# Optimization experiments

Hardware: AMD Instinct MI355X
Metric: run time of the kernel (lower is better)

Reference implementation:

```python
import jax, jax.numpy as jnp
import numpy as np

B = 131072
D = 64          # d_model
T = 4           # num_tiles
TEMP = 0.5


def setup_inputs() -> dict:
    key = jax.random.key(0)
    ks = jax.random.split(key, 16)
    s = 0.02
    return {
        "a_vec": jax.random.normal(ks[0], (B, D), dtype=jnp.float32),
        "b_vec": jax.random.normal(ks[1], (B, D), dtype=jnp.float32),
        "pos_encoding": jax.random.normal(ks[2], (B, 8), dtype=jnp.float32),
        # router: Linear(2D+8 -> D), GELU, Linear(D -> T)
        "Wr1": jax.random.normal(ks[3], (2 * D + 8, D), dtype=jnp.float32) * s,
        "br1": jnp.zeros((D,), dtype=jnp.float32),
        "Wr2": jax.random.normal(ks[4], (D, T), dtype=jnp.float32) * s,
        "br2": jnp.zeros((T,), dtype=jnp.float32),
        # tile nets: per-tile Linear(2D -> 2D), GELU, Linear(2D -> D)
        "W1": jax.random.normal(ks[5], (T, 2 * D, 2 * D), dtype=jnp.float32) * s,
        "b1": jnp.zeros((T, 2 * D), dtype=jnp.float32),
        "W2": jax.random.normal(ks[6], (T, 2 * D, D), dtype=jnp.float32) * s,
        "b2": jnp.zeros((T, D), dtype=jnp.float32),
    }


def _router(x, Wr1, br1, Wr2, br2):
    h = jax.nn.gelu(x @ Wr1 + br1, approximate=False)  # torch nn.GELU is exact
    return (h @ Wr2 + br2) / TEMP


def reference(a_vec, b_vec, pos_encoding, Wr1, br1, Wr2, br2, W1, b1, W2, b2):
    pair = jnp.concatenate([a_vec, b_vec], axis=-1)            # (B, 2D)

    # Routing 1 uses pair; routing 2 uses flipped pair. Both expert passes
    # consume `pair` (faithful to the original code, which feeds pair both times).
    idx1 = jnp.argmax(_router(jnp.concatenate([pair, pos_encoding], -1),
                              Wr1, br1, Wr2, br2), axis=-1)    # (B,)
    pair_flip = jnp.concatenate([b_vec, a_vec], axis=-1)
    idx2 = jnp.argmax(_router(jnp.concatenate([pair_flip, pos_encoding], -1),
                              Wr1, br1, Wr2, br2), axis=-1)    # (B,)

    # Run all tiles on every sample (small T), then gather the routed output.
    h = jax.nn.gelu(jnp.einsum('bi,tij->btj', pair, W1) + b1, approximate=False)  # (B,T,2D)
    out_all = jnp.einsum('bth,thd->btd', h, W2) + b2                              # (B,T,D)

    out1 = jnp.take_along_axis(out_all, idx1[:, None, None], axis=1)[:, 0]
    out2 = jnp.take_along_axis(out_all, idx2[:, None, None], axis=1)[:, 0]
    return out1, out2
```

## Files before the change

kernel.cpp:

```cpp
#include <hip/hip_runtime.h>

#define B_N 131072

using bfrag_t = __attribute__((ext_vector_type(8))) short;
using acc_t   = __attribute__((ext_vector_type(4))) float;
using v4f     = __attribute__((ext_vector_type(4))) float;
using i32x4_t = __attribute__((ext_vector_type(4))) int;

__device__ __forceinline__ unsigned short f2bf(float f) {
  unsigned int u = __float_as_uint(f);
  u += 0x7FFFu + ((u >> 16) & 1u);
  return (unsigned short)(u >> 16);
}

__device__ __forceinline__ unsigned int pk2bf(float x, float y) {
  return (unsigned int)f2bf(x) | ((unsigned int)f2bf(y) << 16);
}

__device__ __forceinline__ void gload_lds16(const void* g, void* l) {
  __builtin_amdgcn_global_load_lds((const __attribute__((address_space(1))) void*)g,
                                   (__attribute__((address_space(3))) void*)l, 16, 0, 0);
}

__device__ __forceinline__ float gelu_f(float x) {
  float ax = fabsf(x) * 0.70710678118654752f;
  float t  = __builtin_amdgcn_rcpf(fmaf(0.3275911f, ax, 1.0f));
  float p  = fmaf(1.061405429f, t, -1.453152027f);
  p = fmaf(p, t, 1.421413741f);
  p = fmaf(p, t, -0.284496736f);
  p = fmaf(p, t, 0.254829592f);
  p = p * t;
  float e  = __expf(-ax * ax);
  float er = fmaf(-p, e, 1.0f);
  er = (x < 0.0f) ? -er : er;
  return 0.5f * x * (1.0f + er);
}

__global__ __launch_bounds__(256) void prepack2_k(
    const float* __restrict__ Wr1, const float* __restrict__ br1,
    const float* __restrict__ Wr2, const float* __restrict__ br2,
    const float* __restrict__ W1, const float* __restrict__ W2,
    float* __restrict__ RW, short* __restrict__ W1s, short* __restrict__ W2s,
    unsigned int* __restrict__ counts) {
  int gt = blockIdx.x * 256 + threadIdx.x;
  if (gt < 4) counts[gt] = 0u;
  for (int idx = gt; idx < 142 * 64; idx += 16384) {
    int row = idx >> 6, j = idx & 63; float val;
    if (row < 136)      val = Wr1[row * 64 + j];
    else if (row == 136) val = br1[j];
    else if (row < 141) val = Wr2[(row - 137) * 64 + j];
    else                val = (j < 4) ? br2[j] : 0.0f;
    RW[idx] = val;
  }
  for (int ch = gt; ch < 8192; ch += 16384) {
    int t = ch >> 11, r = (ch >> 4) & 127, c = ch & 15;
    const float* src = W1 + t * 16384 + r;
    short* dst = W1s + (t * 128 + r) * 128 + ((c ^ (r & 15)) * 8);
    #pragma unroll
    for (int m = 0; m < 8; m++) dst[m] = (short)f2bf(src[(c * 8 + m) * 128]);
  }
  for (int ch = gt; ch < 4096; ch += 16384) {
    int t = ch >> 10, d = (ch >> 4) & 63, c = ch & 15;
    const float* src = W2 + t * 8192 + d;
    short* dst = W2s + (t * 64 + d) * 128 + ((c ^ (d & 15)) * 8);
    #pragma unroll
    for (int m = 0; m < 8; m++) dst[m] = (short)f2bf(src[(c * 8 + m) * 64]);
  }
}

__global__ __launch_bounds__(256) void router7_k(
    const float* __restrict__ a, const float* __restrict__ b,
    const float* __restrict__ pos, const float* __restrict__ RW,
    unsigned char* __restrict__ r1, unsigned char* __restrict__ r2,
    unsigned int* __restrict__ gcounts) {
  __shared__ float SB[17928];
  __shared__ unsigned int hcnt[4];
  const int XA = 9088, XB = 13248, PP = 17408;
  int tid = threadIdx.x, wave = tid >> 6, lane = tid & 63;
  int s0 = blockIdx.x * 64;
  if (tid < 4) hcnt[tid] = 0u;

  for (int it = 0; it < 9; it++) {
    int cb = it * 256 + wave * 64;
    if (cb < 2272) {
      int chunk = cb + lane;
      if (chunk < 2272) gload_lds16(RW + chunk * 4, (char*)SB + cb * 16);
    }
  }
  #pragma unroll
  for (int it = 0; it < 4; it++) {
    int idx = it * 256 + tid;
    int s = idx >> 4, c = idx & 15;
    v4f va = *(const v4f*)(a + (size_t)(s0 + s) * 64 + c * 4);
    v4f vb = *(const v4f*)(b + (size_t)(s0 + s) * 64 + c * 4);
    #pragma unroll
    for (int k = 0; k < 4; k++) {
      SB[XA + (c * 4 + k) * 65 + s] = va[k];
      SB[XB + (c * 4 + k) * 65 + s] = vb[k];
    }
  }
  #pragma unroll
  for (int r = 0; r < 2; r++) {
    int idx = r * 256 + tid;
    int s = idx >> 3, c = idx & 7;
    SB[PP + c * 65 + s] = pos[(size_t)(s0 + s) * 8 + c];
  }
  __syncthreads();

  int sq = tid >> 2, jq = tid & 3;
  v4f acc1[4], acc2[4];
  #pragma unroll
  for (int e = 0; e < 4; e++) {
    v4f bi = *(const v4f*)(SB + 136 * 64 + jq * 16 + e * 4);
    acc1[e] = bi; acc2[e] = bi;
  }
  #pragma unroll 4
  for (int i = 0; i < 64; ++i) {
    float xa = SB[XA + i * 65 + sq];
    float xb = SB[XB + i * 65 + sq];
    const v4f* w = (const v4f*)(SB + i * 64 + jq * 16);
    v4f xav = {xa, xa, xa, xa}, xbv = {xb, xb, xb, xb};
    #pragma unroll
    for (int e = 0; e < 4; e++) {
      v4f wv = w[e];
      acc1[e] = __builtin_elementwise_fma(xav, wv, acc1[e]);
      acc2[e] = __builtin_elementwise_fma(xbv, wv, acc2[e]);
    }
  }
  #pragma unroll 4
  for (int i = 0; i < 64; ++i) {
    float xa = SB[XA + i * 65 + sq];
    float xb = SB[XB + i * 65 + sq];
    const v4f* w = (const v4f*)(SB + (64 + i) * 64 + jq * 16);
    v4f xav = {xa, xa, xa, xa}, xbv = {xb, xb, xb, xb};
    #pragma unroll
    for (int e = 0; e < 4; e++) {
      v4f wv = w[e];
      acc1[e] = __builtin_elementwise_fma(xbv, wv, acc1[e]);
      acc2[e] = __builtin_elementwise_fma(xav, wv, acc2[e]);
    }
  }
  #pragma unroll 2
  for (int i = 0; i < 8; ++i) {
    float p = SB[PP + i * 65 + sq];
    const v4f* w = (const v4f*)(SB + (128 + i) * 64 + jq * 16);
    v4f pv = {p, p, p, p};
    #pragma unroll
    for (int e = 0; e < 4; e++) {
      v4f wv = w[e];
      acc1[e] = __builtin_elementwise_fma(pv, wv, acc1[e]);
      acc2[e] = __builtin_elementwise_fma(pv, wv, acc2[e]);
    }
  }
  #pragma unroll
  for (int e = 0; e < 4; e++) {
    #pragma unroll
    for (int c = 0; c < 4; c++) {
      acc1[e][c] = gelu_f(acc1[e][c]);
      acc2[e][c] = gelu_f(acc2[e][c]);
    }
  }
  __syncthreads();
  #pragma unroll
  for (int e = 0; e < 4; e++) {
    #pragma unroll
    for (int c = 0; c < 4; c++) {
      int j = jq * 16 + e * 4 + c;
      SB[XA + j * 65 + sq] = acc1[e][c];
      SB[XB + j * 65 + sq] = acc2[e][c];
    }
  }
  __syncthreads();
  v4f l1 = *(const v4f*)(SB + 141 * 64);
  v4f l2 = l1;
  #pragma unroll 4
  for (int j = 0; j < 64; ++j) {
    float h1 = SB[XA + j * 65 + sq];
    float h2 = SB[XB + j * 65 + sq];
    v4f w2 = *(const v4f*)(SB + 137 * 64 + j * 4);
    v4f h1v = {h1, h1, h1, h1}, h2v = {h2, h2, h2, h2};
    l1 = __builtin_elementwise_fma(h1v, w2, l1);
    l2 = __builtin_elementwise_fma(h2v, w2, l2);
  }
  int idx1 = 0; float b1v = l1[0];
  if (l1[1] > b1v) { b1v = l1[1]; idx1 = 1; }
  if (l1[2] > b1v) { b1v = l1[2]; idx1 = 2; }
  if (l1[3] > b1v) { b1v = l1[3]; idx1 = 3; }
  int idx2 = 0; float b2v = l2[0];
  if (l2[1] > b2v) { b2v = l2[1]; idx2 = 1; }
  if (l2[2] > b2v) { b2v = l2[2]; idx2 = 2; }
  if (l2[3] > b2v) { b2v = l2[3]; idx2 = 3; }
  if (jq == 0) {
    r1[s0 + sq] = (unsigned char)idx1;
    r2[s0 + sq] = (unsigned char)idx2;
    atomicAdd(&hcnt[idx1], 1u);
    atomicAdd(&hcnt[idx2], 1u);
  }
  __syncthreads();
  if (tid < 4) atomicAdd(&gcounts[tid], hcnt[tid]);
}

__global__ __launch_bounds__(256) void offsets_k(
    const unsigned int* __restrict__ counts, unsigned int* __restrict__ table,
    unsigned int* __restrict__ cursors, unsigned int* __restrict__ list) {
  __shared__ unsigned int ps[5], cnt[4];
  int tid = threadIdx.x;
  if (tid == 0) {
    unsigned int acc = 0;
    for (int t = 0; t < 4; t++) {
      ps[t] = acc;
      unsigned int c = counts[t];
      cnt[t] = c;
      acc += ((c + 127u) >> 7) << 7;
    }
    ps[4] = acc;
    #pragma unroll
    for (int t = 0; t < 5; t++) table[t] = ps[t];
    #pragma unroll
    for (int t = 0; t < 4; t++) cursors[t] = ps[t];
  }
  __syncthreads();
  #pragma unroll
  for (int r = 0; r < 2; r++) {
    int idx = r * 256 + tid;
    int t = idx >> 7, i = idx & 127;
    unsigned int pos = ps[t] + cnt[t] + (unsigned int)i;
    if (pos < ps[t + 1]) list[pos] = 0xFFFFFFFFu;
  }
}

__global__ __launch_bounds__(256) void place_k(
    const unsigned char* __restrict__ r1, const unsigned char* __restrict__ r2,
    unsigned int* __restrict__ cursors, unsigned int* __restrict__ list) {
  __shared__ unsigned int lc[4], lb[4];
  int tid = threadIdx.x;
  if (tid < 4) lc[tid] = 0u;
  __syncthreads();
  int s = blockIdx.x * 256 + tid;
  int e1 = (int)r1[s], e2 = (int)r2[s];
  unsigned int k1 = atomicAdd(&lc[e1], 1u);
  unsigned int k2 = atomicAdd(&lc[e2], 1u);
  __syncthreads();
  if (tid < 4) lb[tid] = atomicAdd(&cursors[tid], lc[tid]);
  __syncthreads();
  list[lb[e1] + k1] = ((unsigned int)s << 1);
  list[lb[e2] + k2] = ((unsigned int)s << 1) | 1u;
}

__global__ __launch_bounds__(256) void expert3_k(
    const float* __restrict__ a, const float* __restrict__ b,
    const short* __restrict__ W1s, const short* __restrict__ W2s,
    const float* __restrict__ b1, const float* __restrict__ b2,
    const unsigned int* __restrict__ table, const unsigned int* __restrict__ list,
    float* __restrict__ out) {
  __shared__ short LB[24576];
  __shared__ unsigned int eLS[128];
  int tid = threadIdx.x;
  int wave = tid >> 6, lane = tid & 63;
  int q = lane >> 4, sm = lane & 15;

  unsigned int p0 = blockIdx.x * 128u;
  unsigned int t1 = table[1], t2 = table[2], t3 = table[3], t4 = table[4];
  if (p0 >= t4) return;
  int t = (p0 >= t1) + (p0 >= t2) + (p0 >= t3);

  if (tid < 128) eLS[tid] = list[p0 + tid];
  __syncthreads();

  #pragma unroll
  for (int r = 0; r < 8; r++) {
    int slot = r * 256 + tid;
    int g = slot >> 10, sg = slot & 1023;
    int f = sg >> 6, l = sg & 63;
    int sgrp = f >> 2, kb = f & 3;
    int ls2 = g * 64 + sgrp * 16 + (l & 15);
    unsigned int e = eLS[ls2];
    int s = (e == 0xFFFFFFFFu) ? 0 : (int)(e >> 1);
    int k = kb * 32 + (l >> 4) * 8;
    const float* src = (k < 64) ? (a + (size_t)s * 64 + k) : (b + (size_t)s * 64 + (k - 64));
    acc_t v0 = *(const acc_t*)(src);
    acc_t v1 = *(const acc_t*)(src + 4);
    i32x4_t pk;
    pk[0] = (int)pk2bf(v0[0], v0[1]);
    pk[1] = (int)pk2bf(v0[2], v0[3]);
    pk[2] = (int)pk2bf(v1[0], v1[1]);
    pk[3] = (int)pk2bf(v1[2], v1[3]);
    *(i32x4_t*)(&LB[slot * 8]) = pk;
  }
  __syncthreads();
  bfrag_t bfrag[2][4];
  #pragma unroll
  for (int g = 0; g < 2; g++)
    #pragma unroll
    for (int kb = 0; kb < 4; kb++)
      bfrag[g][kb] = *(const bfrag_t*)(&LB[((g * 16 + wave * 4 + kb) * 64 + lane) * 8]);

  unsigned int eA = eLS[wave * 16 + sm];
  unsigned int eB = eLS[64 + wave * 16 + sm];
  __syncthreads();

  acc_t zero = {0.f, 0.f, 0.f, 0.f};
  int vb[4];
  #pragma unroll
  for (int kb = 0; kb < 4; kb++) vb[kb] = sm * 256 + (((kb * 4 + q) ^ sm) * 16);
  int addr0 = (((q & 1) * 2) * 16 + sm) * 4;
  int addr1 = addr0 + 64;
  bool hi = (q >> 1) != 0;

  #pragma unroll
  for (int it = 0; it < 12; it++) {
    int cb = it * 256 + wave * 64;
    int chunk = cb + lane;
    const short* gsrc = (chunk < 2048) ? (W1s + t * 16384 + chunk * 8)
                                       : (W2s + t * 8192 + (chunk - 2048) * 8);
    gload_lds16(gsrc, (char*)LB + cb * 16);
  }
  __syncthreads();

  #pragma unroll
  for (int g = 0; g < 2; g++) {
    unsigned int hp[8][2];
    #pragma unroll
    for (int mt = 0; mt < 8; mt++) {
      acc_t c = zero;
      #pragma unroll
      for (int kb = 0; kb < 4; kb++) {
        bfrag_t A = *(const bfrag_t*)((const char*)LB + mt * 4096 + vb[kb]);
        c = __builtin_amdgcn_mfma_f32_16x16x32_bf16(A, bfrag[g][kb], c, 0, 0, 0);
      }
      acc_t bv = *(const acc_t*)(b1 + t * 128 + mt * 16 + q * 4);
      float g0 = gelu_f(c[0] + bv[0]);
      float g1 = gelu_f(c[1] + bv[1]);
      float g2 = gelu_f(c[2] + bv[2]);
      float g3 = gelu_f(c[3] + bv[3]);
      hp[mt][0] = pk2bf(g0, g1);
      hp[mt][1] = pk2bf(g2, g3);
    }
    bfrag_t b2f[4];
    #pragma unroll
    for (int kb2 = 0; kb2 < 4; kb2++) {
      int p00 = __builtin_amdgcn_ds_bpermute(addr0, (int)hp[2 * kb2][0]);
      int p01 = __builtin_amdgcn_ds_bpermute(addr0, (int)hp[2 * kb2][1]);
      int p10 = __builtin_amdgcn_ds_bpermute(addr1, (int)hp[2 * kb2][0]);
      int p11 = __builtin_amdgcn_ds_bpermute(addr1, (int)hp[2 * kb2][1]);
      int q00 = __builtin_amdgcn_ds_bpermute(addr0, (int)hp[2 * kb2 + 1][0]);
      int q01 = __builtin_amdgcn_ds_bpermute(addr0, (int)hp[2 * kb2 + 1][1]);
      int q10 = __builtin_amdgcn_ds_bpermute(addr1, (int)hp[2 * kb2 + 1][0]);
      int q11 = __builtin_amdgcn_ds_bpermute(addr1, (int)hp[2 * kb2 + 1][1]);
      i32x4_t w;
      w[0] = hi ? q00 : p00;
      w[1] = hi ? q01 : p01;
      w[2] = hi ? q10 : p10;
      w[3] = hi ? q11 : p11;
      b2f[kb2] = __builtin_bit_cast(bfrag_t, w);
    }
    unsigned int e = g ? eB : eA;
    bool live = (e != 0xFFFFFFFFu);
    size_t so = ((size_t)(e & 1u)) * B_N + (size_t)(e >> 1);
    float* p = out + so * 64 + q * 4;
    #pragma unroll
    for (int mt2 = 0; mt2 < 4; mt2++) {
      acc_t c = zero;
      #pragma unroll
      for (int kb2 = 0; kb2 < 4; kb2++) {
        bfrag_t A = *(const bfrag_t*)((const char*)LB + 32768 + mt2 * 4096 + vb[kb2]);
        c = __builtin_amdgcn_mfma_f32_16x16x32_bf16(A, b2f[kb2], c, 0, 0, 0);
      }
      acc_t bv = *(const acc_t*)(b2 + t * 64 + mt2 * 16 + q * 4);
      c[0] += bv[0]; c[1] += bv[1]; c[2] += bv[2]; c[3] += bv[3];
      if (live) *(acc_t*)(p + mt2 * 16) = c;
    }
  }
}

extern "C" void kernel_launch(void* const* d_in, const int* in_sizes, int n_in,
                              void* d_out, int out_size, void* d_ws, size_t ws_size,
                              hipStream_t stream) {
  const float* a   = (const float*)d_in[0];
  const float* bv  = (const float*)d_in[1];
  const float* pos = (const float*)d_in[2];
  const float* Wr1 = (const float*)d_in[3];
  const float* br1 = (const float*)d_in[4];
  const float* Wr2 = (const float*)d_in[5];
  const float* br2 = (const float*)d_in[6];
  const float* W1  = (const float*)d_in[7];
  const float* b1  = (const float*)d_in[8];
  const float* W2  = (const float*)d_in[9];
  const float* b2  = (const float*)d_in[10];
  float* out = (float*)d_out;

  unsigned char* r1 = (unsigned char*)d_ws;
  unsigned char* r2 = r1 + B_N;
  float* RW  = (float*)((char*)d_ws + 262144);
  short* W1s = (short*)((char*)d_ws + 298496);
  short* W2s = (short*)((char*)d_ws + 429568);
  unsigned int* counts  = (unsigned int*)((char*)d_ws + 495104);
  unsigned int* cursors = (unsigned int*)((char*)d_ws + 495120);
  unsigned int* table   = (unsigned int*)((char*)d_ws + 495136);
  unsigned int* list    = (unsigned int*)((char*)d_ws + 495168);

  prepack2_k<<<64, 256, 0, stream>>>(Wr1, br1, Wr2, br2, W1, W2, RW, W1s, W2s, counts);
  router7_k<<<B_N / 64, 256, 0, stream>>>(a, bv, pos, RW, r1, r2, counts);
  offsets_k<<<1, 256, 0, stream>>>(counts, table, cursors, list);
  place_k<<<B_N / 256, 256, 0, stream>>>(r1, r2, cursors, list);
  expert3_k<<<2052, 256, 0, stream>>>(a, bv, W1s, W2s, b1, b2, table, list, out);
}
```

Measured before the change: 254.2 us.

## Restructure router: per-wave column slices with scalar weight loads, smaller LDS

The router kernel no longer stages the router weights in shared memory. Each wave owns a 16-column slice of the hidden layer, so its weight reads are wave-uniform and can go through scalar loads. Each lane handles one sample, with inputs kept row-major in LDS using a padded stride. This roughly halves LDS use to allow more resident blocks (launch bounds 4), and replaces the shared-memory atomic histogram with wave ballots plus popcount. The trade-offs are more registers per thread (32 accumulators) and every wave redundantly computing the second-layer logits.

```diff
diff --git a/kernel.cpp b/kernel.cpp
--- a/kernel.cpp
+++ b/kernel.cpp
@@ -68,119 +68,107 @@
   }
 }
 
-__global__ __launch_bounds__(256) void router7_k(
+__global__ __launch_bounds__(256, 4) void router8_k(
     const float* __restrict__ a, const float* __restrict__ b,
     const float* __restrict__ pos, const float* __restrict__ RW,
     unsigned char* __restrict__ r1, unsigned char* __restrict__ r2,
     unsigned int* __restrict__ gcounts) {
-  __shared__ float SB[17928];
-  __shared__ unsigned int hcnt[4];
-  const int XA = 9088, XB = 13248, PP = 17408;
-  int tid = threadIdx.x, wave = tid >> 6, lane = tid & 63;
+  __shared__ float SB[8832];
+  int tid = threadIdx.x, lane = tid & 63;
   int s0 = blockIdx.x * 64;
-  if (tid < 4) hcnt[tid] = 0u;
-
-  for (int it = 0; it < 9; it++) {
-    int cb = it * 256 + wave * 64;
-    if (cb < 2272) {
-      int chunk = cb + lane;
-      if (chunk < 2272) gload_lds16(RW + chunk * 4, (char*)SB + cb * 16);
-    }
-  }
-  #pragma unroll
-  for (int it = 0; it < 4; it++) {
+
+  #pragma unroll
+  for (int it = 0; it < 8; it++) {
     int idx = it * 256 + tid;
-    int s = idx >> 4, c = idx & 15;
-    v4f va = *(const v4f*)(a + (size_t)(s0 + s) * 64 + c * 4);
-    v4f vb = *(const v4f*)(b + (size_t)(s0 + s) * 64 + c * 4);
-    #pragma unroll
-    for (int k = 0; k < 4; k++) {
-      SB[XA + (c * 4 + k) * 65 + s] = va[k];
-      SB[XB + (c * 4 + k) * 65 + s] = vb[k];
-    }
+    int s = idx >> 5, c = idx & 31;
+    const float* src = (c < 16) ? (a + (size_t)(s0 + s) * 64 + c * 4)
+                                : (b + (size_t)(s0 + s) * 64 + (c - 16) * 4);
+    v4f v = *(const v4f*)src;
+    float* dst = SB + s * 129 + c * 4;
+    dst[0] = v[0]; dst[1] = v[1]; dst[2] = v[2]; dst[3] = v[3];
   }
   #pragma unroll
   for (int r = 0; r < 2; r++) {
     int idx = r * 256 + tid;
     int s = idx >> 3, c = idx & 7;
-    SB[PP + c * 65 + s] = pos[(size_t)(s0 + s) * 8 + c];
-  }
-  __syncthreads();
-
-  int sq = tid >> 2, jq = tid & 3;
-  v4f acc1[4], acc2[4];
-  #pragma unroll
-  for (int e = 0; e < 4; e++) {
-    v4f bi = *(const v4f*)(SB + 136 * 64 + jq * 16 + e * 4);
-    acc1[e] = bi; acc2[e] = bi;
+    SB[8256 + s * 9 + c] = pos[(size_t)(s0 + s) * 8 + c];
+  }
+  __syncthreads();
+
+  int wch = __builtin_amdgcn_readfirstlane(tid >> 6) * 16;
+  const float* Wb = RW + wch;
+  float acc1[16], acc2[16];
+  #pragma unroll
+  for (int c = 0; c < 16; c++) {
+    float bi = RW[136 * 64 + wch + c];
+    acc1[c] = bi; acc2[c] = bi;
+  }
+  const float* Xrow = SB + lane * 129;
+  #pragma unroll 2
+  for (int i = 0; i < 64; i++) {
+    float xa = Xrow[i];
+    float xb = Xrow[64 + i];
+    const float* w = Wb + i * 64;
+    #pragma unroll
+    for (int c = 0; c < 16; c++) {
+      float wv = w[c];
+      acc1[c] = fmaf(xa, wv, acc1[c]);
+      acc2[c] = fmaf(xb, wv, acc2[c]);
+    }
+  }
+  #pragma unroll 2
+  for (int i = 0; i < 64; i++) {
+    float xa = Xrow[i];
+    float xb = Xrow[64 + i];
+    const float* w = Wb + (64 + i) * 64;
+    #pragma unroll
+    for (int c = 0; c < 16; c++) {
+      float wv = w[c];
+      acc1[c] = fmaf(xb, wv, acc1[c]);
+      acc2[c] = fmaf(xa, wv, acc2[c]);
+    }
+  }
+  const float* Prow = SB + 8256 + lane * 9;
+  #pragma unroll 2
+  for (int i = 0; i < 8; i++) {
+    float p = Prow[i];
+    const float* w = Wb + (128 + i) * 64;
+    #pragma unroll
+    for (int c = 0; c < 16; c++) {
+      float wv = w[c];
+      acc1[c] = fmaf(p, wv, acc1[c]);
+      acc2[c] = fmaf(p, wv, acc2[c]);
+    }
+  }
+  #pragma unroll
+  for (int c = 0; c < 16; c++) {
+    acc1[c] = gelu_f(acc1[c]);
+    acc2[c] = gelu_f(acc2[c]);
+  }
+  __syncthreads();
+  #pragma unroll
+  for (int c = 0; c < 16; c++) {
+    SB[lane * 65 + wch + c] = acc1[c];
+    SB[4160 + lane * 65 + wch + c] = acc2[c];
+  }
+  __syncthreads();
+  float l1[4], l2[4];
+  #pragma unroll
+  for (int m = 0; m < 4; m++) {
+    float bi = RW[141 * 64 + m];
+    l1[m] = bi; l2[m] = bi;
   }
   #pragma unroll 4
-  for (int i = 0; i < 64; ++i) {
-    float xa = SB[XA + i * 65 + sq];
-    float xb = SB[XB + i * 65 + sq];
-    const v4f* w = (const v4f*)(SB + i * 64 + jq * 16);
-    v4f xav = {xa, xa, xa, xa}, xbv = {xb, xb, xb, xb};
-    #pragma unroll
-    for (int e = 0; e < 4; e++) {
-      v4f wv = w[e];
-      acc1[e] = __builtin_elementwise_fma(xav, wv, acc1[e]);
-      acc2[e] = __builtin_elementwise_fma(xbv, wv, acc2[e]);
-    }
-  }
-  #pragma unroll 4
-  for (int i = 0; i < 64; ++i) {
-    float xa = SB[XA + i * 65 + sq];
-    float xb = SB[XB + i * 65 + sq];
-    const v4f* w = (const v4f*)(SB + (64 + i) * 64 + jq * 16);
-    v4f xav = {xa, xa, xa, xa}, xbv = {xb, xb, xb, xb};
-    #pragma unroll
-    for (int e = 0; e < 4; e++) {
-      v4f wv = w[e];
-      acc1[e] = __builtin_elementwise_fma(xbv, wv, acc1[e]);
-      acc2[e] = __builtin_elementwise_fma(xav, wv, acc2[e]);
-    }
-  }
-  #pragma unroll 2
-  for (int i = 0; i < 8; ++i) {
-    float p = SB[PP + i * 65 + sq];
-    const v4f* w = (const v4f*)(SB + (128 + i) * 64 + jq * 16);
-    v4f pv = {p, p, p, p};
-    #pragma unroll
-    for (int e = 0; e < 4; e++) {
-      v4f wv = w[e];
-      acc1[e] = __builtin_elementwise_fma(pv, wv, acc1[e]);
-      acc2[e] = __builtin_elementwise_fma(pv, wv, acc2[e]);
-    }
-  }
-  #pragma unroll
-  for (int e = 0; e < 4; e++) {
-    #pragma unroll
-    for (int c = 0; c < 4; c++) {
-      acc1[e][c] = gelu_f(acc1[e][c]);
-      acc2[e][c] = gelu_f(acc2[e][c]);
-    }
-  }
-  __syncthreads();
-  #pragma unroll
-  for (int e = 0; e < 4; e++) {
-    #pragma unroll
-    for (int c = 0; c < 4; c++) {
-      int j = jq * 16 + e * 4 + c;
-      SB[XA + j * 65 + sq] = acc1[e][c];
-      SB[XB + j * 65 + sq] = acc2[e][c];
-    }
-  }
-  __syncthreads();
-  v4f l1 = *(const v4f*)(SB + 141 * 64);
-  v4f l2 = l1;
-  #pragma unroll 4
-  for (int j = 0; j < 64; ++j) {
-    float h1 = SB[XA + j * 65 + sq];
-    float h2 = SB[XB + j * 65 + sq];
-    v4f w2 = *(const v4f*)(SB + 137 * 64 + j * 4);
-    v4f h1v = {h1, h1, h1, h1}, h2v = {h2, h2, h2, h2};
-    l1 = __builtin_elementwise_fma(h1v, w2, l1);
-    l2 = __builtin_elementwise_fma(h2v, w2, l2);
+  for (int j = 0; j < 64; j++) {
+    float h1 = SB[lane * 65 + j];
+    float h2 = SB[4160 + lane * 65 + j];
+    const float* w2 = RW + 137 * 64 + j * 4;
+    #pragma unroll
+    for (int m = 0; m < 4; m++) {
+      float wv = w2[m];
+      l1[m] = fmaf(h1, wv, l1[m]);
+      l2[m] = fmaf(h2, wv, l2[m]);
+    }
   }
   int idx1 = 0; float b1v = l1[0];
   if (l1[1] > b1v) { b1v = l1[1]; idx1 = 1; }
@@ -190,14 +178,17 @@
   if (l2[1] > b2v) { b2v = l2[1]; idx2 = 1; }
   if (l2[2] > b2v) { b2v = l2[2]; idx2 = 2; }
   if (l2[3] > b2v) { b2v = l2[3]; idx2 = 3; }
-  if (jq == 0) {
-    r1[s0 + sq] = (unsigned char)idx1;
-    r2[s0 + sq] = (unsigned char)idx2;
-    atomicAdd(&hcnt[idx1], 1u);
-    atomicAdd(&hcnt[idx2], 1u);
-  }
-  __syncthreads();
-  if (tid < 4) atomicAdd(&gcounts[tid], hcnt[tid]);
+  if (tid < 64) {
+    r1[s0 + lane] = (unsigned char)idx1;
+    r2[s0 + lane] = (unsigned char)idx2;
+    #pragma unroll
+    for (int t = 0; t < 4; t++) {
+      unsigned long long m1 = __ballot(idx1 == t);
+      unsigned long long m2 = __ballot(idx2 == t);
+      if (lane == 0)
+        atomicAdd(gcounts + t, (unsigned int)(__popcll(m1) + __popcll(m2)));
+    }
+  }
 }
 
 __global__ __launch_bounds__(256) void offsets_k(
@@ -400,7 +391,7 @@
   unsigned int* list    = (unsigned int*)((char*)d_ws + 495168);
 
   prepack2_k<<<64, 256, 0, stream>>>(Wr1, br1, Wr2, br2, W1, W2, RW, W1s, W2s, counts);
-  router7_k<<<B_N / 64, 256, 0, stream>>>(a, bv, pos, RW, r1, r2, counts);
+  router8_k<<<B_N / 64, 256, 0, stream>>>(a, bv, pos, RW, r1, r2, counts);
   offsets_k<<<1, 256, 0, stream>>>(counts, table, cursors, list);
   place_k<<<B_N / 256, 256, 0, stream>>>(r1, r2, cursors, list);
   expert3_k<<<2052, 256, 0, stream>>>(a, bv, W1s, W2s, b1, b2, table, list, out);
```

Result: slower. 304.3 us (+19.7%).
